# Performance work log

Measured on AMD Instinct MI355X. Metric: run time of the kernel, lower is better.

Reference implementation:

```python
import jax, jax.numpy as jnp
import numpy as np


def setup_inputs() -> dict:
    key = jax.random.key(0)
    N, D = 262144, 64
    x = jax.random.normal(key, (N, D), dtype=jnp.float32)
    return {"x": x, "n_clusters": 256, "n_iter": 10}


def reference(x, n_clusters, n_iter):
    # Faithful KMeans.fit: centroids init = first K rows; each iter assigns
    # points to nearest centroid (squared L2) then recomputes centroids via
    # per-cluster mean (bincount scatter-reduce in the original).
    N, D = x.shape
    K = n_clusters
    c0 = x[:K, :]
    x_sq = jnp.sum(x * x, axis=1)  # [N], reused every iteration

    def step(carry, _):
        c, _ = carry
        # squared distances ||x - c||^2 expanded: same math as ((x_i - c_j)**2).sum(-1)
        c_sq = jnp.sum(c * c, axis=1)                      # [K]
        d = x_sq[:, None] - 2.0 * (x @ c.T) + c_sq[None, :]  # [N, K]
        cl = jnp.argmin(d, axis=1)                          # [N] labels vs OLD centroids
        ones = jnp.ones((N,), dtype=x.dtype)
        Ncl = jax.ops.segment_sum(ones, cl, num_segments=K)  # bincount(cl)
        sums = jax.ops.segment_sum(x, cl, num_segments=K)    # per-dim weighted bincount
        new_c = sums / Ncl[:, None]
        return (new_c, cl), None

    cl0 = jnp.zeros((N,), dtype=jnp.int32)
    (c, cl), _ = jax.lax.scan(step, (c0, cl0), None, length=n_iter)
    return c, cl
```

## Files before the change

### kernel.cpp

```cpp
#include <hip/hip_runtime.h>
#include <hip/hip_bf16.h>

#define KC 256
#define DIM 64
#define NITER 10
#define CPAD 66

typedef __attribute__((ext_vector_type(16))) float f32x16;
typedef __attribute__((ext_vector_type(4)))  float f32x4;
typedef __attribute__((ext_vector_type(8)))  short bf16x8;

__device__ __forceinline__ float np_pairwise_sq64(const float* a) {
    float r[8];
#pragma unroll
    for (int j = 0; j < 8; ++j) r[j] = __fmul_rn(a[j], a[j]);
#pragma unroll
    for (int i = 8; i < 64; i += 8)
#pragma unroll
        for (int j = 0; j < 8; ++j)
            r[j] = __fadd_rn(r[j], __fmul_rn(a[i + j], a[i + j]));
    float t01 = __fadd_rn(r[0], r[1]), t23 = __fadd_rn(r[2], r[3]);
    float t45 = __fadd_rn(r[4], r[5]), t67 = __fadd_rn(r[6], r[7]);
    return __fadd_rn(__fadd_rn(t01, t23), __fadd_rn(t45, t67));
}

__device__ __forceinline__ unsigned short f2bf(float f) {
    __hip_bfloat16 h = __float2bfloat16(f);
    return *reinterpret_cast<unsigned short*>(&h);
}

__global__ void init_k(const float* __restrict__ x, float* __restrict__ c) {
    const int idx = blockIdx.x * 256 + threadIdx.x;
    if (idx < KC * DIM) c[idx] = x[idx];
}

__global__ __launch_bounds__(256) void xinit_k(
    const float* __restrict__ x, unsigned short* __restrict__ xbf,
    float* __restrict__ xsq_g, int n)
{
    const int i = blockIdx.x * 256 + threadIdx.x;
    if (i >= n) return;
    float xr[DIM];
    const float4* xv = reinterpret_cast<const float4*>(x + (size_t)i * DIM);
    unsigned short* xb = xbf + (size_t)i * DIM;
#pragma unroll
    for (int j = 0; j < DIM / 4; ++j) {
        float4 v = xv[j];
        xr[4 * j + 0] = v.x; xr[4 * j + 1] = v.y;
        xr[4 * j + 2] = v.z; xr[4 * j + 3] = v.w;
        xb[4 * j + 0] = f2bf(v.x); xb[4 * j + 1] = f2bf(v.y);
        xb[4 * j + 2] = f2bf(v.z); xb[4 * j + 3] = f2bf(v.w);
    }
    xsq_g[i] = np_pairwise_sq64(xr);
}

__global__ __launch_bounds__(256) void csqg_k(
    const float* __restrict__ c, float* __restrict__ csq_g, int* __restrict__ nan_g)
{
    const int k = threadIdx.x;
    if (k == 0) *nan_g = 0x7fffffff;
    __syncthreads();
    float cr[DIM];
    const float4* cp = reinterpret_cast<const float4*>(c + k * DIM);
#pragma unroll
    for (int j = 0; j < DIM / 4; ++j) {
        float4 v = cp[j];
        cr[4 * j + 0] = v.x; cr[4 * j + 1] = v.y;
        cr[4 * j + 2] = v.z; cr[4 * j + 3] = v.w;
    }
    const float s = np_pairwise_sq64(cr);
    csq_g[k] = s;
    if (s != s) atomicMin(nan_g, k);
}

__global__ __launch_bounds__(256) void csqg2_k(
    const float* __restrict__ c, float* __restrict__ csq_g, int* __restrict__ nan_g,
    unsigned short* __restrict__ cbf, float* __restrict__ csqmax_g)
{
    __shared__ float smax[256];
    const int k = threadIdx.x;
    if (k == 0) *nan_g = 0x7fffffff;
    __syncthreads();
    float cr[DIM];
    const float4* cp = reinterpret_cast<const float4*>(c + k * DIM);
    unsigned short* cb = cbf + (size_t)k * DIM;
#pragma unroll
    for (int j = 0; j < DIM / 4; ++j) {
        float4 v = cp[j];
        cr[4 * j + 0] = v.x; cr[4 * j + 1] = v.y;
        cr[4 * j + 2] = v.z; cr[4 * j + 3] = v.w;
        cb[4 * j + 0] = f2bf(v.x); cb[4 * j + 1] = f2bf(v.y);
        cb[4 * j + 2] = f2bf(v.z); cb[4 * j + 3] = f2bf(v.w);
    }
    const float s = np_pairwise_sq64(cr);
    csq_g[k] = s;
    if (s != s) atomicMin(nan_g, k);
    smax[k] = (s == s) ? s : 0.0f;
    __syncthreads();
    for (int d = 128; d >= 1; d >>= 1) {
        if (k < d) smax[k] = fmaxf(smax[k], smax[k + d]);
        __syncthreads();
    }
    if (k == 0) *csqmax_g = smax[0];
}

__global__ __launch_bounds__(256) void assign_mfma_k(
    const float* __restrict__ x, const unsigned short* __restrict__ xbf,
    const float* __restrict__ xsq_g, const float* __restrict__ c,
    const unsigned short* __restrict__ cbf, const float* __restrict__ csq_g,
    const float* __restrict__ csqmax_g, const int* __restrict__ nan_g,
    float* __restrict__ labels, int* __restrict__ hist, int n)
{
    __shared__ unsigned short c_lds[128 * CPAD];
    __shared__ float csq_lds[KC];
    __shared__ int u_shm[1024];
    __shared__ int ccnt[256];

    short* cand = reinterpret_cast<short*>(u_shm);
    const int t = threadIdx.x;
    const int p0 = blockIdx.x * 256;

    csq_lds[t] = csq_g[t];
    ccnt[t] = 0;
    const float csqmax = *csqmax_g;
    const int firstNan = *nan_g;

    const int w = t >> 6, l = t & 63;
    const int grp = l >> 4, lr = l & 15;

    float rm[4][4];
#pragma unroll
    for (int q = 0; q < 4; ++q)
#pragma unroll
        for (int p = 0; p < 4; ++p) rm[q][p] = 3.4e38f;

#pragma unroll
    for (int h = 0; h < 2; ++h) {
        __syncthreads();
        for (int idx = t; idx < 128 * 8; idx += 256) {
            const int row = idx >> 3, ch = idx & 7;
            *reinterpret_cast<bf16x8*>(&c_lds[row * CPAD + ch * 8]) =
                *reinterpret_cast<const bf16x8*>(cbf + (size_t)(h * 128 + row) * DIM + ch * 8);
        }
        __syncthreads();
#pragma unroll
        for (int q = 0; q < 4; ++q) {
            const int pbase = p0 + w * 64 + q * 16;
            const unsigned short* xb = xbf + (size_t)(pbase + lr) * DIM;
            const bf16x8 a0 = *reinterpret_cast<const bf16x8*>(xb + grp * 8);
            const bf16x8 a1 = *reinterpret_cast<const bf16x8*>(xb + 32 + grp * 8);
            const int prow = pbase + grp * 4;
            const float xs0 = xsq_g[prow + 0], xs1 = xsq_g[prow + 1];
            const float xs2 = xsq_g[prow + 2], xs3 = xsq_g[prow + 3];
#pragma unroll
            for (int ct = 0; ct < 8; ++ct) {
                const unsigned short* cb = &c_lds[(ct * 16 + lr) * CPAD];
                const bf16x8 b0 = *reinterpret_cast<const bf16x8*>(cb + grp * 8);
                const bf16x8 b1 = *reinterpret_cast<const bf16x8*>(cb + 32 + grp * 8);
                f32x4 acc = {0.f, 0.f, 0.f, 0.f};
                acc = __builtin_amdgcn_mfma_f32_16x16x32_bf16(a0, b0, acc, 0, 0, 0);
                acc = __builtin_amdgcn_mfma_f32_16x16x32_bf16(a1, b1, acc, 0, 0, 0);
                const float cs = csq_lds[h * 128 + ct * 16 + lr];
                rm[q][0] = fminf(rm[q][0], __fadd_rn(fmaf(-2.0f, acc[0], xs0), cs));
                rm[q][1] = fminf(rm[q][1], __fadd_rn(fmaf(-2.0f, acc[1], xs1), cs));
                rm[q][2] = fminf(rm[q][2], __fadd_rn(fmaf(-2.0f, acc[2], xs2), cs));
                rm[q][3] = fminf(rm[q][3], __fadd_rn(fmaf(-2.0f, acc[3], xs3), cs));
            }
        }
    }

#pragma unroll
    for (int q = 0; q < 4; ++q) {
#pragma unroll
        for (int m = 1; m < 16; m <<= 1) {
            rm[q][0] = fminf(rm[q][0], __shfl_xor(rm[q][0], m, 64));
            rm[q][1] = fminf(rm[q][1], __shfl_xor(rm[q][1], m, 64));
            rm[q][2] = fminf(rm[q][2], __shfl_xor(rm[q][2], m, 64));
            rm[q][3] = fminf(rm[q][3], __shfl_xor(rm[q][3], m, 64));
        }
    }

#pragma unroll
    for (int h = 0; h < 2; ++h) {
        __syncthreads();
        for (int idx = t; idx < 128 * 8; idx += 256) {
            const int row = idx >> 3, ch = idx & 7;
            *reinterpret_cast<bf16x8*>(&c_lds[row * CPAD + ch * 8]) =
                *reinterpret_cast<const bf16x8*>(cbf + (size_t)(h * 128 + row) * DIM + ch * 8);
        }
        __syncthreads();
#pragma unroll
        for (int q = 0; q < 4; ++q) {
            const int pbase = p0 + w * 64 + q * 16;
            const unsigned short* xb = xbf + (size_t)(pbase + lr) * DIM;
            const bf16x8 a0 = *reinterpret_cast<const bf16x8*>(xb + grp * 8);
            const bf16x8 a1 = *reinterpret_cast<const bf16x8*>(xb + 32 + grp * 8);
            const int prow = pbase + grp * 4;
            const float xs0 = xsq_g[prow + 0], xs1 = xsq_g[prow + 1];
            const float xs2 = xsq_g[prow + 2], xs3 = xsq_g[prow + 3];
            const float th0 = rm[q][0] + 2.0f * (0.00399f * sqrtf(xs0 * csqmax) + 0.02f);
            const float th1 = rm[q][1] + 2.0f * (0.00399f * sqrtf(xs1 * csqmax) + 0.02f);
            const float th2 = rm[q][2] + 2.0f * (0.00399f * sqrtf(xs2 * csqmax) + 0.02f);
            const float th3 = rm[q][3] + 2.0f * (0.00399f * sqrtf(xs3 * csqmax) + 0.02f);
            const int pidx0 = w * 64 + q * 16 + grp * 4;
#pragma unroll
            for (int ct = 0; ct < 8; ++ct) {
                const unsigned short* cb = &c_lds[(ct * 16 + lr) * CPAD];
                const bf16x8 b0 = *reinterpret_cast<const bf16x8*>(cb + grp * 8);
                const bf16x8 b1 = *reinterpret_cast<const bf16x8*>(cb + 32 + grp * 8);
                f32x4 acc = {0.f, 0.f, 0.f, 0.f};
                acc = __builtin_amdgcn_mfma_f32_16x16x32_bf16(a0, b0, acc, 0, 0, 0);
                acc = __builtin_amdgcn_mfma_f32_16x16x32_bf16(a1, b1, acc, 0, 0, 0);
                const int kcol = h * 128 + ct * 16 + lr;
                const float cs = csq_lds[kcol];
                const float d0 = __fadd_rn(fmaf(-2.0f, acc[0], xs0), cs);
                const float d1 = __fadd_rn(fmaf(-2.0f, acc[1], xs1), cs);
                const float d2 = __fadd_rn(fmaf(-2.0f, acc[2], xs2), cs);
                const float d3 = __fadd_rn(fmaf(-2.0f, acc[3], xs3), cs);
                if (d0 <= th0) { int s = atomicAdd(&ccnt[pidx0 + 0], 1); if (s < 8) cand[(pidx0 + 0) * 8 + s] = (short)kcol; }
                if (d1 <= th1) { int s = atomicAdd(&ccnt[pidx0 + 1], 1); if (s < 8) cand[(pidx0 + 1) * 8 + s] = (short)kcol; }
                if (d2 <= th2) { int s = atomicAdd(&ccnt[pidx0 + 2], 1); if (s < 8) cand[(pidx0 + 2) * 8 + s] = (short)kcol; }
                if (d3 <= th3) { int s = atomicAdd(&ccnt[pidx0 + 3], 1); if (s < 8) cand[(pidx0 + 3) * 8 + s] = (short)kcol; }
            }
        }
    }
    __syncthreads();

    const int i = p0 + t;
    const bool valid = (i < n);
    int lbl = 0;
    if (valid) {
        const int nc = ccnt[t];
        if (firstNan != 0x7fffffff) {
            lbl = firstNan;
        } else if (nc == 1) {
            lbl = (int)cand[t * 8];
        } else {
            const float xsqv = xsq_g[i];
            const float4* xrow = reinterpret_cast<const float4*>(x + (size_t)i * DIM);
            float bd = 3.4e38f;
            int bk = 0;
            const bool fullscan = (nc == 0) || (nc > 8);
            const int lim = fullscan ? KC : nc;
            for (int s = 0; s < lim; ++s) {
                const int k = fullscan ? s : (int)cand[t * 8 + s];
                const float4* crow = reinterpret_cast<const float4*>(c + (size_t)k * DIM);
                float acc = 0.0f;
#pragma unroll
                for (int db = 0; db < 16; ++db) {
                    const float4 a = xrow[db], b = crow[db];
                    acc = fmaf(a.x, b.x, acc); acc = fmaf(a.y, b.y, acc);
                    acc = fmaf(a.z, b.z, acc); acc = fmaf(a.w, b.w, acc);
                }
                const float dd = __fadd_rn(fmaf(-2.0f, acc, xsqv), csq_lds[k]);
                if (dd < bd) { bd = dd; bk = k; }
                else if (dd == bd && k < bk) bk = k;
            }
            lbl = bk;
        }
        labels[i] = (float)lbl;
    }
    __syncthreads();

    int* whist = u_shm;
    for (int j = t; j < 4 * KC; j += 256) whist[j] = 0;
    __syncthreads();
    const int lane = t & 63, wv = t >> 6;
    unsigned long long same = __ballot(valid);
#pragma unroll
    for (int bit = 0; bit < 8; ++bit) {
        unsigned long long bb = __ballot((lbl >> bit) & 1);
        same &= ((lbl >> bit) & 1) ? bb : ~bb;
    }
    if (valid && lane == __builtin_ctzll(same))
        whist[wv * KC + lbl] = (int)__popcll(same);
    __syncthreads();
    if (t < KC)
        hist[(size_t)blockIdx.x * KC + t] =
            whist[t] + whist[KC + t] + whist[2 * KC + t] + whist[3 * KC + t];
}

__global__ __launch_bounds__(256) void assign_hist_k(
    const float* __restrict__ x, const float* __restrict__ c,
    const float* __restrict__ csq_g, const int* __restrict__ nan_g,
    float* __restrict__ labels, int* __restrict__ hist, int n)
{
    __shared__ int whist[4 * KC];
    const int t = threadIdx.x;
    for (int j = t; j < 4 * KC; j += 256) whist[j] = 0;

    const int i = blockIdx.x * 256 + t;
    const bool valid = (i < n);

    float xr[DIM];
    const float4* xv = reinterpret_cast<const float4*>(x + (size_t)(valid ? i : 0) * DIM);
#pragma unroll
    for (int j = 0; j < DIM / 4; ++j) {
        float4 v = xv[j];
        xr[4 * j + 0] = v.x; xr[4 * j + 1] = v.y;
        xr[4 * j + 2] = v.z; xr[4 * j + 3] = v.w;
    }
    const float xsq = np_pairwise_sq64(xr);
    const int firstNan = *nan_g;

    float best = __int_as_float(0x7f800000);
    int bk = 0;

#pragma unroll 1
    for (int k = 0; k < KC; ++k) {
        f32x16 h0, h1, h2, h3;
        float cs;
        const float* rp = c + (size_t)k * DIM;
        asm volatile("s_load_dwordx16 %0, %1, 0x0"  : "=s"(h0) : "s"(rp));
        asm volatile("s_load_dwordx16 %0, %1, 0x40" : "=s"(h1) : "s"(rp));
        asm volatile("s_load_dwordx16 %0, %1, 0x80" : "=s"(h2) : "s"(rp));
        asm volatile("s_load_dwordx16 %0, %1, 0xc0" : "=s"(h3) : "s"(rp));
        asm volatile("s_load_dword %0, %1, 0x0"     : "=s"(cs) : "s"(csq_g + k));
        asm volatile("s_waitcnt lgkmcnt(0)"
                     : "+s"(h0), "+s"(h1), "+s"(h2), "+s"(h3), "+s"(cs));
        __builtin_amdgcn_sched_barrier(0);

        float acc = 0.0f;
#pragma unroll
        for (int d = 0; d < 16; ++d) acc = fmaf(xr[d],      h0[d], acc);
#pragma unroll
        for (int d = 0; d < 16; ++d) acc = fmaf(xr[16 + d], h1[d], acc);
#pragma unroll
        for (int d = 0; d < 16; ++d) acc = fmaf(xr[32 + d], h2[d], acc);
#pragma unroll
        for (int d = 0; d < 16; ++d) acc = fmaf(xr[48 + d], h3[d], acc);

        const float dist = __fadd_rn(fmaf(-2.0f, acc, xsq), cs);
        if (dist < best) { best = dist; bk = k; }
    }

    int lbl = 0;
    if (valid) {
        lbl = (firstNan != 0x7fffffff) ? firstNan : bk;
        labels[i] = (float)lbl;
    }

    __syncthreads();
    const int lane = t & 63, w = t >> 6;
    unsigned long long same = __ballot(valid);
#pragma unroll
    for (int bit = 0; bit < 8; ++bit) {
        unsigned long long bb = __ballot((lbl >> bit) & 1);
        same &= ((lbl >> bit) & 1) ? bb : ~bb;
    }
    if (valid && lane == __builtin_ctzll(same))
        whist[w * KC + lbl] = (int)__popcll(same);
    __syncthreads();
    if (t < KC)
        hist[(size_t)blockIdx.x * KC + t] =
            whist[t] + whist[KC + t] + whist[2 * KC + t] + whist[3 * KC + t];
}

__global__ __launch_bounds__(256) void scan1_k(
    int* __restrict__ hist, int nb, int* __restrict__ cnt)
{
    __shared__ int sbuf[256];
    const int k = blockIdx.x;
    const int t = threadIdx.x;
    const int epb = (nb + 255) / 256;
    const int b0 = t * epb;

    int s = 0;
    for (int u = 0; u < epb; ++u) {
        const int b = b0 + u;
        if (b < nb) s += hist[(size_t)b * KC + k];
    }
    sbuf[t] = s;
    __syncthreads();
    int incl = s;
#pragma unroll
    for (int d = 1; d < 256; d <<= 1) {
        const int v = (t >= d) ? sbuf[t - d] : 0;
        __syncthreads();
        incl += v;
        sbuf[t] = incl;
        __syncthreads();
    }
    int run = incl - s;
    for (int u = 0; u < epb; ++u) {
        const int b = b0 + u;
        if (b < nb) {
            const int v = hist[(size_t)b * KC + k];
            hist[(size_t)b * KC + k] = run;
            run += v;
        }
    }
    if (t == 255) cnt[k] = incl;
}

__global__ __launch_bounds__(256) void scan2_k(
    const int* __restrict__ cnt, int* __restrict__ base)
{
    __shared__ int sbuf[256];
    const int t = threadIdx.x;
    const int padded = (cnt[t] + 63) & ~63;
    sbuf[t] = padded;
    __syncthreads();
    int incl = padded;
#pragma unroll
    for (int d = 1; d < 256; d <<= 1) {
        const int v = (t >= d) ? sbuf[t - d] : 0;
        __syncthreads();
        incl += v;
        sbuf[t] = incl;
        __syncthreads();
    }
    base[t] = incl - padded;
}

__global__ __launch_bounds__(256) void scatter_k(
    const float* __restrict__ labels, const int* __restrict__ hist,
    const int* __restrict__ base, int* __restrict__ order, int n)
{
    __shared__ int whist[4 * KC];
    const int t = threadIdx.x;
    for (int j = t; j < 4 * KC; j += 256) whist[j] = 0;
    __syncthreads();

    const int i = blockIdx.x * 256 + t;
    const bool valid = (i < n);
    const int lbl = valid ? (int)labels[i] : 0;
    const int lane = t & 63, w = t >> 6;

    unsigned long long same = __ballot(valid);
#pragma unroll
    for (int bit = 0; bit < 8; ++bit) {
        unsigned long long bb = __ballot((lbl >> bit) & 1);
        same &= ((lbl >> bit) & 1) ? bb : ~bb;
    }
    const unsigned long long below = (1ull << lane) - 1ull;
    const int rank_wave = (int)__popcll(same & below);
    if (valid && lane == __builtin_ctzll(same))
        whist[w * KC + lbl] = (int)__popcll(same);
    __syncthreads();

    if (valid) {
        int off = rank_wave;
        for (int ww = 0; ww < w; ++ww) off += whist[ww * KC + lbl];
        const int pos = base[lbl] + hist[(size_t)blockIdx.x * KC + lbl] + off;
        order[pos] = i;
    }
}

__global__ __launch_bounds__(256) void permute_k(
    const float* __restrict__ x, const int* __restrict__ order,
    float* __restrict__ xs)
{
    const int r = blockIdx.x * 4 + (threadIdx.x >> 6);
    const int d = threadIdx.x & 63;
    const int idx = order[r];
    float v = 0.0f;
    if (idx >= 0) v = x[(size_t)idx * DIM + d];
    xs[(size_t)r * DIM + d] = v;
}

#define SUMBR 128

__global__ __launch_bounds__(512) void sum4_k(
    const float* __restrict__ xs, const int* __restrict__ base,
    const int* __restrict__ cnt, float* __restrict__ c)
{
    __shared__ float sbuf[2][SUMBR * DIM];

    const int k = blockIdx.x;
    const int t = threadIdx.x;
    const int w = t >> 6;
    const int lane = t & 63;
    const int b0 = base[k];
    const int ct = cnt[k];
    const int ctp = (ct + 63) & ~63;
    const int nbt = (ctp + SUMBR - 1) / SUMBR;

    const f32x4* src4 = reinterpret_cast<const f32x4*>(xs + (size_t)b0 * DIM);

    if (w < 7 && nbt > 0) {
        const int bs4 = ((ctp < SUMBR) ? ctp : SUMBR) * 16;
        f32x4* dst4 = reinterpret_cast<f32x4*>(sbuf[0]);
        for (int idx = t; idx < bs4; idx += 448)
            dst4[idx] = src4[idx];
    }
    __syncthreads();

    float acc = 0.0f;
    for (int b = 0; b < nbt; ++b) {
        if (w < 7) {
            if (b + 1 < nbt) {
                const int jb = (b + 1) * SUMBR;
                const int rows = ((ctp - jb) < SUMBR) ? (ctp - jb) : SUMBR;
                const int bs4 = rows * 16;
                f32x4* dst4 = reinterpret_cast<f32x4*>(sbuf[(b + 1) & 1]);
                for (int idx = t; idx < bs4; idx += 448)
                    dst4[idx] = src4[(size_t)jb * 16 + idx];
            }
        } else {
            const int jb = b * SUMBR;
            const int rows = ((ctp - jb) < SUMBR) ? (ctp - jb) : SUMBR;
            const float* sb = &sbuf[b & 1][lane];
            for (int r = 0; r < rows; ++r)
                acc = __fadd_rn(acc, sb[(size_t)r * DIM]);
        }
        __syncthreads();
    }

    if (w == 7)
        c[k * DIM + lane] = __fdiv_rn(acc, (float)ct);
}

__global__ __launch_bounds__(64) void gather_k(
    const float* __restrict__ x, const int* __restrict__ order,
    const int* __restrict__ base, const int* __restrict__ cnt,
    float* __restrict__ c)
{
    const int k = blockIdx.x;
    const int lane = threadIdx.x;
    const int b0 = base[k];
    const int ct = cnt[k];
    float acc = 0.0f;
    int j = 0;
    for (; j + 32 <= ct; j += 32) {
        float v[32];
#pragma unroll
        for (int u = 0; u < 32; ++u)
            v[u] = x[(size_t)order[b0 + j + u] * DIM + lane];
#pragma unroll
        for (int u = 0; u < 32; ++u) acc = __fadd_rn(acc, v[u]);
    }
    for (; j < ct; ++j)
        acc = __fadd_rn(acc, x[(size_t)order[b0 + j] * DIM + lane]);
    c[k * DIM + lane] = __fdiv_rn(acc, (float)ct);
}

extern "C" void kernel_launch(void* const* d_in, const int* in_sizes, int n_in,
                              void* d_out, int out_size, void* d_ws, size_t ws_size,
                              hipStream_t stream)
{
    const float* x = (const float*)d_in[0];
    const int n = in_sizes[0] / DIM;

    float* out_c = (float*)d_out;
    float* out_labels = out_c + KC * DIM;

    const int nb = (n + 255) / 256;
    const int nstride = n + KC * 64;

    size_t off = 0;
    auto alloc = [&](size_t bytes) -> size_t {
        size_t o = off; off = (off + bytes + 255) & ~(size_t)255; return o;
    };
    char*  w        = (char*)d_ws;
    float* csq_g    = (float*)(w + alloc(KC * sizeof(float)));
    int*   nan_g    = (int*)(w + alloc(256));
    float* csqmax_g = (float*)(w + alloc(256));
    unsigned short* cbf_g = (unsigned short*)(w + alloc(KC * DIM * sizeof(unsigned short)));
    int*   hist  = (int*)(w + alloc((size_t)nb * KC * sizeof(int)));
    int*   base  = (int*)(w + alloc(KC * sizeof(int)));
    int*   cnt   = (int*)(w + alloc(KC * sizeof(int)));
    int*   order = (int*)(w + alloc((size_t)nstride * sizeof(int)));
    const size_t med_need = off;
    float* xs    = (float*)(w + alloc((size_t)nstride * DIM * sizeof(float)));
    const size_t big_need = off;
    unsigned short* xbf = (unsigned short*)(w + alloc((size_t)n * DIM * sizeof(unsigned short)));
    float* xsq_g = (float*)(w + alloc((size_t)n * sizeof(float)));
    const size_t huge_need = off;

    const bool med  = (ws_size >= med_need);
    const bool big  = (ws_size >= big_need);
    const bool huge = (ws_size >= huge_need);

    init_k<<<(KC * DIM + 255) / 256, 256, 0, stream>>>(x, out_c);
    if (huge)
        xinit_k<<<nb, 256, 0, stream>>>(x, xbf, xsq_g, n);

    for (int it = 0; it < NITER; ++it) {
        if (huge) {
            csqg2_k<<<1, 256, 0, stream>>>(out_c, csq_g, nan_g, cbf_g, csqmax_g);
            assign_mfma_k<<<nb, 256, 0, stream>>>(x, xbf, xsq_g, out_c, cbf_g,
                                                  csq_g, csqmax_g, nan_g,
                                                  out_labels, hist, n);
        } else {
            csqg_k<<<1, 256, 0, stream>>>(out_c, csq_g, nan_g);
            assign_hist_k<<<nb, 256, 0, stream>>>(x, out_c, csq_g, nan_g,
                                                  out_labels, hist, n);
        }
        if (med) {
            scan1_k<<<KC, 256, 0, stream>>>(hist, nb, cnt);
            scan2_k<<<1, 256, 0, stream>>>(cnt, base);
            if (big) {
                (void)hipMemsetAsync(order, 0xFF, (size_t)nstride * sizeof(int), stream);
                scatter_k<<<nb, 256, 0, stream>>>(out_labels, hist, base, order, n);
                permute_k<<<nstride / 4, 256, 0, stream>>>(x, order, xs);
                sum4_k<<<KC, 512, 0, stream>>>(xs, base, cnt, out_c);
            } else {
                scatter_k<<<nb, 256, 0, stream>>>(out_labels, hist, base, order, n);
                gather_k<<<KC, 64, 0, stream>>>(x, order, base, cnt, out_c);
            }
        }
    }
}
```

Baseline: 1.766 ms.

## Interleave sorted points by groups of four and stream-sum with deep inline-asm prefetch

Cluster segments are now padded to multiples of 96 rows. The permute kernel writes rows interleaved in groups of four, so each lane holds a float4 containing one dimension across four consecutive points. The per-cluster sum becomes a single-wave kernel that keeps 24 outstanding dwordx4 global loads in flight through hand-written waitcnt pipelining, replacing the LDS double-buffered 512-thread reducer. This targets the latency-bound per-cluster reduction, but it reduces parallelism to 64 threads per cluster and depends on inline asm and the compiler honouring the vmcnt accounting.

```diff
diff --git a/kernel.cpp b/kernel.cpp
--- a/kernel.cpp
+++ b/kernel.cpp
@@ -398,7 +398,7 @@
 {
     __shared__ int sbuf[256];
     const int t = threadIdx.x;
-    const int padded = (cnt[t] + 63) & ~63;
+    const int padded = ((cnt[t] + 95) / 96) * 96;
     sbuf[t] = padded;
     __syncthreads();
     int incl = padded;
@@ -447,68 +447,81 @@
     }
 }
 
-__global__ __launch_bounds__(256) void permute_k(
+__global__ __launch_bounds__(256) void permute2_k(
     const float* __restrict__ x, const int* __restrict__ order,
-    float* __restrict__ xs)
-{
-    const int r = blockIdx.x * 4 + (threadIdx.x >> 6);
-    const int d = threadIdx.x & 63;
-    const int idx = order[r];
-    float v = 0.0f;
-    if (idx >= 0) v = x[(size_t)idx * DIM + d];
-    xs[(size_t)r * DIM + d] = v;
-}
-
-#define SUMBR 128
-
-__global__ __launch_bounds__(512) void sum4_k(
-    const float* __restrict__ xs, const int* __restrict__ base,
+    float* __restrict__ xs2)
+{
+    __shared__ float tile[4][4][65];
+    const int t = threadIdx.x;
+    const int w = t >> 6, l = t & 63;
+    const int j = blockIdx.x * 4 + w;
+    const int g = l >> 4, m = l & 15;
+
+    const int idx = order[4 * j + g];
+    float4 v = make_float4(0.f, 0.f, 0.f, 0.f);
+    if (idx >= 0) v = *reinterpret_cast<const float4*>(x + (size_t)idx * DIM + m * 4);
+    tile[w][g][m * 4 + 0] = v.x;
+    tile[w][g][m * 4 + 1] = v.y;
+    tile[w][g][m * 4 + 2] = v.z;
+    tile[w][g][m * 4 + 3] = v.w;
+    float4 o;
+    o.x = tile[w][0][l]; o.y = tile[w][1][l];
+    o.z = tile[w][2][l]; o.w = tile[w][3][l];
+    *reinterpret_cast<float4*>(xs2 + (size_t)j * 256 + l * 4) = o;
+}
+
+#define SLOT_ISSUE(i) { asm volatile("global_load_dwordx4 %0, %1, off" \
+                          : "=v"(A##i) : "v"(addr)); addr += 1024ull; }
+#define SLOT_ADDS(i)  { acc = __fadd_rn(acc, A##i.x); acc = __fadd_rn(acc, A##i.y); \
+                        acc = __fadd_rn(acc, A##i.z); acc = __fadd_rn(acc, A##i.w); }
+#define SLOT_STEP(i)  { asm volatile("s_waitcnt vmcnt(23)" : "+v"(A##i)); \
+                        __builtin_amdgcn_sched_barrier(0); SLOT_ADDS(i) SLOT_ISSUE(i) }
+#define SLOT_DRAIN(i, cnt) { asm volatile("s_waitcnt vmcnt(" #cnt ")" : "+v"(A##i)); \
+                        __builtin_amdgcn_sched_barrier(0); SLOT_ADDS(i) }
+
+__global__ __launch_bounds__(64) void sum6_k(
+    const float* __restrict__ xs2, const int* __restrict__ base,
     const int* __restrict__ cnt, float* __restrict__ c)
 {
-    __shared__ float sbuf[2][SUMBR * DIM];
-
     const int k = blockIdx.x;
-    const int t = threadIdx.x;
-    const int w = t >> 6;
-    const int lane = t & 63;
+    const int lane = threadIdx.x;
     const int b0 = base[k];
     const int ct = cnt[k];
-    const int ctp = (ct + 63) & ~63;
-    const int nbt = (ctp + SUMBR - 1) / SUMBR;
-
-    const f32x4* src4 = reinterpret_cast<const f32x4*>(xs + (size_t)b0 * DIM);
-
-    if (w < 7 && nbt > 0) {
-        const int bs4 = ((ctp < SUMBR) ? ctp : SUMBR) * 16;
-        f32x4* dst4 = reinterpret_cast<f32x4*>(sbuf[0]);
-        for (int idx = t; idx < bs4; idx += 448)
-            dst4[idx] = src4[idx];
-    }
-    __syncthreads();
+    const int ctp = ((ct + 95) / 96) * 96;
+    const int T = ctp >> 2;
 
     float acc = 0.0f;
-    for (int b = 0; b < nbt; ++b) {
-        if (w < 7) {
-            if (b + 1 < nbt) {
-                const int jb = (b + 1) * SUMBR;
-                const int rows = ((ctp - jb) < SUMBR) ? (ctp - jb) : SUMBR;
-                const int bs4 = rows * 16;
-                f32x4* dst4 = reinterpret_cast<f32x4*>(sbuf[(b + 1) & 1]);
-                for (int idx = t; idx < bs4; idx += 448)
-                    dst4[idx] = src4[(size_t)jb * 16 + idx];
-            }
-        } else {
-            const int jb = b * SUMBR;
-            const int rows = ((ctp - jb) < SUMBR) ? (ctp - jb) : SUMBR;
-            const float* sb = &sbuf[b & 1][lane];
-            for (int r = 0; r < rows; ++r)
-                acc = __fadd_rn(acc, sb[(size_t)r * DIM]);
-        }
-        __syncthreads();
-    }
-
-    if (w == 7)
-        c[k * DIM + lane] = __fdiv_rn(acc, (float)ct);
+    if (T > 0) {
+        unsigned long long addr =
+            (unsigned long long)(const void*)(xs2 + (size_t)(b0 >> 2) * 256 + lane * 4);
+        f32x4 A0, A1, A2, A3, A4, A5, A6, A7, A8, A9, A10, A11;
+        f32x4 A12, A13, A14, A15, A16, A17, A18, A19, A20, A21, A22, A23;
+
+        SLOT_ISSUE(0)  SLOT_ISSUE(1)  SLOT_ISSUE(2)  SLOT_ISSUE(3)
+        SLOT_ISSUE(4)  SLOT_ISSUE(5)  SLOT_ISSUE(6)  SLOT_ISSUE(7)
+        SLOT_ISSUE(8)  SLOT_ISSUE(9)  SLOT_ISSUE(10) SLOT_ISSUE(11)
+        SLOT_ISSUE(12) SLOT_ISSUE(13) SLOT_ISSUE(14) SLOT_ISSUE(15)
+        SLOT_ISSUE(16) SLOT_ISSUE(17) SLOT_ISSUE(18) SLOT_ISSUE(19)
+        SLOT_ISSUE(20) SLOT_ISSUE(21) SLOT_ISSUE(22) SLOT_ISSUE(23)
+
+        const int nsteps = T / 24 - 1;
+        for (int s2 = 0; s2 < nsteps; ++s2) {
+            SLOT_STEP(0)  SLOT_STEP(1)  SLOT_STEP(2)  SLOT_STEP(3)
+            SLOT_STEP(4)  SLOT_STEP(5)  SLOT_STEP(6)  SLOT_STEP(7)
+            SLOT_STEP(8)  SLOT_STEP(9)  SLOT_STEP(10) SLOT_STEP(11)
+            SLOT_STEP(12) SLOT_STEP(13) SLOT_STEP(14) SLOT_STEP(15)
+            SLOT_STEP(16) SLOT_STEP(17) SLOT_STEP(18) SLOT_STEP(19)
+            SLOT_STEP(20) SLOT_STEP(21) SLOT_STEP(22) SLOT_STEP(23)
+        }
+
+        SLOT_DRAIN(0, 23)  SLOT_DRAIN(1, 22)  SLOT_DRAIN(2, 21)  SLOT_DRAIN(3, 20)
+        SLOT_DRAIN(4, 19)  SLOT_DRAIN(5, 18)  SLOT_DRAIN(6, 17)  SLOT_DRAIN(7, 16)
+        SLOT_DRAIN(8, 15)  SLOT_DRAIN(9, 14)  SLOT_DRAIN(10, 13) SLOT_DRAIN(11, 12)
+        SLOT_DRAIN(12, 11) SLOT_DRAIN(13, 10) SLOT_DRAIN(14, 9)  SLOT_DRAIN(15, 8)
+        SLOT_DRAIN(16, 7)  SLOT_DRAIN(17, 6)  SLOT_DRAIN(18, 5)  SLOT_DRAIN(19, 4)
+        SLOT_DRAIN(20, 3)  SLOT_DRAIN(21, 2)  SLOT_DRAIN(22, 1)  SLOT_DRAIN(23, 0)
+    }
+    c[k * DIM + lane] = __fdiv_rn(acc, (float)ct);
 }
 
 __global__ __launch_bounds__(64) void gather_k(
@@ -546,7 +559,7 @@
     float* out_labels = out_c + KC * DIM;
 
     const int nb = (n + 255) / 256;
-    const int nstride = n + KC * 64;
+    const int nstride = n + KC * 96;
 
     size_t off = 0;
     auto alloc = [&](size_t bytes) -> size_t {
@@ -562,7 +575,7 @@
     int*   cnt   = (int*)(w + alloc(KC * sizeof(int)));
     int*   order = (int*)(w + alloc((size_t)nstride * sizeof(int)));
     const size_t med_need = off;
-    float* xs    = (float*)(w + alloc((size_t)nstride * DIM * sizeof(float)));
+    float* xs2   = (float*)(w + alloc((size_t)nstride * DIM * sizeof(float)));
     const size_t big_need = off;
     unsigned short* xbf = (unsigned short*)(w + alloc((size_t)n * DIM * sizeof(unsigned short)));
     float* xsq_g = (float*)(w + alloc((size_t)n * sizeof(float)));
@@ -593,8 +606,8 @@
             if (big) {
                 (void)hipMemsetAsync(order, 0xFF, (size_t)nstride * sizeof(int), stream);
                 scatter_k<<<nb, 256, 0, stream>>>(out_labels, hist, base, order, n);
-                permute_k<<<nstride / 4, 256, 0, stream>>>(x, order, xs);
-                sum4_k<<<KC, 512, 0, stream>>>(xs, base, cnt, out_c);
+                permute2_k<<<nstride / 16, 256, 0, stream>>>(x, order, xs2);
+                sum6_k<<<KC, 64, 0, stream>>>(xs2, base, cnt, out_c);
             } else {
                 scatter_k<<<nb, 256, 0, stream>>>(out_labels, hist, base, order, n);
                 gather_k<<<KC, 64, 0, stream>>>(x, order, base, cnt, out_c);
```

New measurement: 1.447 ms. -18.1%, faster.
